# Performance work log

Hardware: AMD Instinct MI355X
Metric: run time of the kernel (lower is better)

Reference implementation:

```python
import jax, jax.numpy as jnp
import numpy as np

N_NODES = 100000
N_EDGES = 3200000
N_GRAPHS = 1024
IN_DIM, HID, OUT = 1, 32, 32
BN_EPS = 1e-5


def setup_inputs() -> dict:
    key = jax.random.key(0)
    ks = jax.random.split(key, 12)
    inp = {
        "x": jax.random.normal(ks[0], (N_NODES, IN_DIM), dtype=jnp.float32),
        "edge_index": jax.random.randint(ks[1], (2, N_EDGES), 0, N_NODES, dtype=jnp.int64),
        "batch": jnp.sort(jax.random.randint(ks[2], (N_NODES,), 0, N_GRAPHS, dtype=jnp.int64)),
        # GCNConv linear weights (out = x @ W + b) and BatchNorm (eval-mode) params
        "W1": jax.random.normal(ks[3], (IN_DIM, HID), dtype=jnp.float32) / np.sqrt(IN_DIM),
        "b1": jnp.zeros((HID,), jnp.float32),
        "bn1_g": jnp.ones((HID,), jnp.float32),
        "bn1_b": jnp.zeros((HID,), jnp.float32),
        "bn1_m": jax.random.normal(ks[4], (HID,), dtype=jnp.float32) * 0.1,
        "bn1_v": jnp.ones((HID,), jnp.float32),
        "W2": jax.random.normal(ks[5], (HID, HID), dtype=jnp.float32) / np.sqrt(HID),
        "b2": jnp.zeros((HID,), jnp.float32),
        "bn2_g": jnp.ones((HID,), jnp.float32),
        "bn2_b": jnp.zeros((HID,), jnp.float32),
        "bn2_m": jax.random.normal(ks[6], (HID,), dtype=jnp.float32) * 0.1,
        "bn2_v": jnp.ones((HID,), jnp.float32),
        "W3": jax.random.normal(ks[7], (HID, OUT), dtype=jnp.float32) / np.sqrt(HID),
        "b3": jnp.zeros((OUT,), jnp.float32),
    }
    return inp


def _gcn_norm(edge_index, n_nodes):
    # add self loops, compute sym-normalized edge weights (PyG GCNConv default)
    loop = jnp.arange(n_nodes, dtype=edge_index.dtype)
    src = jnp.concatenate([edge_index[0], loop])
    dst = jnp.concatenate([edge_index[1], loop])
    deg = jax.ops.segment_sum(jnp.ones_like(dst, dtype=jnp.float32), dst, num_segments=n_nodes)
    dinv = jnp.where(deg > 0, jax.lax.rsqrt(deg), 0.0)
    norm = dinv[src] * dinv[dst]  # [E + N]
    return src, dst, norm


def _gcn_conv(x, src, dst, norm, W, b, n_nodes):
    h = x @ W                                   # [N, F_out]
    msg = h[src] * norm[:, None]                # gather + scale, [E+N, F_out]
    out = jax.ops.segment_sum(msg, dst, num_segments=n_nodes)  # scatter-add
    return out + b


def _bn_eval(x, g, b, m, v):
    return (x - m) * jax.lax.rsqrt(v + BN_EPS) * g + b


def reference(x, edge_index, batch, W1, b1, bn1_g, bn1_b, bn1_m, bn1_v,
              W2, b2, bn2_g, bn2_b, bn2_m, bn2_v, W3, b3):
    n = x.shape[0]
    src, dst, norm = _gcn_norm(edge_index, n)
    h = _gcn_conv(x, src, dst, norm, W1, b1, n)
    h = jax.nn.relu(_bn_eval(h, bn1_g, bn1_b, bn1_m, bn1_v))  # dropout = id (eval)
    h = _gcn_conv(h, src, dst, norm, W2, b2, n)
    h = jax.nn.relu(_bn_eval(h, bn2_g, bn2_b, bn2_m, bn2_v))
    h = _gcn_conv(h, src, dst, norm, W3, b3, n)
    # global mean pool over graphs
    sums = jax.ops.segment_sum(h, batch, num_segments=N_GRAPHS)
    cnts = jax.ops.segment_sum(jnp.ones((n,), h.dtype), batch, num_segments=N_GRAPHS)
    return sums / jnp.maximum(cnts, 1.0)[:, None]
```

## Files before the change

kernel.cpp:

```cpp
#include <hip/hip_runtime.h>

#define N_NODES 100000
#define N_EDGES 3200000
#define N_GRAPHS 1024
#define HID 32
#define BN_EPS 1e-5f
#define NB 256

#define NBKT 512
#define NPB 196
#define PART_TILE 4096
#define PART_THREADS 256
#define PART_EPT (PART_TILE / PART_THREADS)


__device__ __forceinline__ int lbound(const int* __restrict__ a, int n, int key) {
    int lo = 0, hi = n;
    while (lo < hi) {
        int mid = (lo + hi) >> 1;
        if (a[mid] < key) lo = mid + 1; else hi = mid;
    }
    return lo;
}

__device__ __forceinline__ float bf2f(unsigned short h) {
    return __uint_as_float((unsigned)h << 16);
}
__device__ __forceinline__ unsigned short f2bf(float x) {
    unsigned u = __float_as_uint(x);
    u += 0x7fffu + ((u >> 16) & 1u);
    return (unsigned short)(u >> 16);
}


__global__ void k_zero(int* __restrict__ bhist) {
    bhist[threadIdx.x] = 0;
}

__global__ void k_hist(const int* __restrict__ dst, int* __restrict__ bhist) {
    __shared__ int h[NBKT];
    for (int i = threadIdx.x; i < NBKT; i += NB) h[i] = 0;
    __syncthreads();
    for (int e = blockIdx.x * NB + threadIdx.x; e < N_EDGES; e += gridDim.x * NB)
        atomicAdd(&h[__builtin_nontemporal_load(&dst[e]) / NPB], 1);
    __syncthreads();
    for (int i = threadIdx.x; i < NBKT; i += NB)
        if (h[i]) atomicAdd(&bhist[i], h[i]);
}

__global__ void k_scan512(const int* __restrict__ bhist, int* __restrict__ bstart,
                          int* __restrict__ bcursor) {
    __shared__ int sm[NBKT];
    int t = threadIdx.x;
    int orig = bhist[t];
    sm[t] = orig;
    __syncthreads();
    for (int off = 1; off < NBKT; off <<= 1) {
        int v = (t >= off) ? sm[t - off] : 0;
        __syncthreads();
        sm[t] += v;
        __syncthreads();
    }
    int ex = sm[t] - orig;
    bstart[t] = ex;
    bcursor[t] = ex;
    if (t == NBKT - 1) bstart[NBKT] = sm[t];
}

__global__ void k_partition(const int* __restrict__ src, const int* __restrict__ dst,
                            int* __restrict__ bcursor, unsigned* __restrict__ ebuf) {
    __shared__ int lh[NBKT];
    __shared__ int lcur[NBKT];
    const int tile0 = blockIdx.x * PART_TILE;
    for (int i = threadIdx.x; i < NBKT; i += PART_THREADS) lh[i] = 0;
    __syncthreads();
    int s[PART_EPT], bk[PART_EPT], dl[PART_EPT];
#pragma unroll
    for (int k = 0; k < PART_EPT; ++k) {
        int e = tile0 + k * PART_THREADS + threadIdx.x;
        bool ok = (e < N_EDGES);
        int sv = ok ? __builtin_nontemporal_load(&src[e]) : 0;
        int dv = ok ? __builtin_nontemporal_load(&dst[e]) : 0;
        s[k] = sv;
        bk[k] = ok ? (dv / NPB) : -1;
        dl[k] = dv - bk[k] * NPB;
        if (ok) atomicAdd(&lh[bk[k]], 1);
    }
    __syncthreads();
    for (int i = threadIdx.x; i < NBKT; i += PART_THREADS)
        lcur[i] = lh[i] ? atomicAdd(&bcursor[i], lh[i]) : 0;
    __syncthreads();
#pragma unroll
    for (int k = 0; k < PART_EPT; ++k) {
        if (bk[k] >= 0) {
            int pos = atomicAdd(&lcur[bk[k]], 1);
            ebuf[pos] = ((unsigned)dl[k] << 17) | (unsigned)s[k];
        }
    }
}

__global__ void k_bucket(const int* __restrict__ bstart,
                         const unsigned* __restrict__ ebuf,
                         const float* __restrict__ x,
                         int* __restrict__ rowstart, int* __restrict__ deg,
                         float* __restrict__ dinv, float* __restrict__ zs1,
                         int* __restrict__ csr) {
    __shared__ int hist[NPB];
    __shared__ int sm[256];
    __shared__ int lcur[NPB];
    const int b = blockIdx.x;
    const int node0 = b * NPB;
    const int nn = N_NODES - node0;
    const int elo = bstart[b], ehi = bstart[b + 1];
    const int t = threadIdx.x;

    for (int i = t; i < NPB; i += blockDim.x) hist[i] = 0;
    __syncthreads();
    for (int e = elo + t; e < ehi; e += blockDim.x)
        atomicAdd(&hist[ebuf[e] >> 17], 1);
    __syncthreads();
    int orig = 0;
    if (t < 256) { orig = (t < NPB) ? hist[t] : 0; sm[t] = orig; }
    __syncthreads();
    for (int off = 1; off < 256; off <<= 1) {
        int v = 0;
        if (t < 256 && t >= off) v = sm[t - off];
        __syncthreads();
        if (t < 256) sm[t] += v;
        __syncthreads();
    }
    if (t < NPB) {
        int ex = sm[t] - orig;
        lcur[t] = ex;
        if (t < nn) {
            int node = node0 + t;
            rowstart[node] = elo + ex;
            deg[node] = orig;
            float di = rsqrtf((float)(orig + 1));
            dinv[node] = di;
            zs1[node] = di * x[node];
        }
    }
    __syncthreads();
    for (int e = elo + t; e < ehi; e += blockDim.x) {
        unsigned pk = ebuf[e];
        int pos = atomicAdd(&lcur[pk >> 17], 1);
        csr[elo + pos] = (int)(pk & 0x1FFFFu);
    }
}


__global__ void k_gather1(const int* __restrict__ rowstart, const int* __restrict__ deg,
                          const int* __restrict__ csr, const float* __restrict__ dinv,
                          const float* __restrict__ zs1, float2* __restrict__ sd) {
    int v = blockIdx.x * NB + threadIdx.x;
    if (v < N_NODES) {
        int lo = rowstart[v], n = deg[v];
        float acc = zs1[v];
        int j = 0;
        for (; j + 4 <= n; j += 4) {
            int u0 = __builtin_nontemporal_load(&csr[lo + j]);
            int u1 = __builtin_nontemporal_load(&csr[lo + j + 1]);
            int u2 = __builtin_nontemporal_load(&csr[lo + j + 2]);
            int u3 = __builtin_nontemporal_load(&csr[lo + j + 3]);
            float a0 = zs1[u0], a1 = zs1[u1], a2 = zs1[u2], a3 = zs1[u3];
            acc += (a0 + a1) + (a2 + a3);
        }
        for (; j < n; ++j) acc += zs1[csr[lo + j]];
        float di = dinv[v];
        sd[v] = make_float2(di * acc, di);
    }
}

__global__ void k_gather2(const int* __restrict__ rowstart, const int* __restrict__ deg,
                          const int* __restrict__ csr, const float2* __restrict__ sd,
                          const float* __restrict__ W1, const float* __restrict__ b1,
                          const float* __restrict__ g1, const float* __restrict__ bb1,
                          const float* __restrict__ m1, const float* __restrict__ v1,
                          const float* __restrict__ W2,
                          const float* __restrict__ b2, const float* __restrict__ g2,
                          const float* __restrict__ bb2, const float* __restrict__ m2,
                          const float* __restrict__ v2, unsigned short* __restrict__ zs3h) {
    __shared__ float Ws[HID * HID];
    __shared__ float rowbuf[NB / HID][HID + 1];
    for (int k = threadIdx.x; k < HID * HID; k += NB) Ws[k] = W2[k];

    int t = blockIdx.x * NB + threadIdx.x;
    int v = t >> 5, f = t & 31, r = threadIdx.x >> 5;
    float sc1 = g1[f] * rsqrtf(v1[f] + BN_EPS);
    float A = W1[f] * sc1;
    float Bc = (b1[f] - m1[f]) * sc1 + bb1[f];
    float acc = 0.0f, di = 0.0f;
    if (v < N_NODES) {
        float2 pv = sd[v];
        di = pv.y;
        acc = di * fmaxf(pv.x * A + Bc, 0.0f);
        int lo = rowstart[v], n = deg[v];
        int j = 0;
        for (; j + 8 <= n; j += 8) {
            int u0 = __builtin_nontemporal_load(&csr[lo + j]);
            int u1 = __builtin_nontemporal_load(&csr[lo + j + 1]);
            int u2 = __builtin_nontemporal_load(&csr[lo + j + 2]);
            int u3 = __builtin_nontemporal_load(&csr[lo + j + 3]);
            int u4 = __builtin_nontemporal_load(&csr[lo + j + 4]);
            int u5 = __builtin_nontemporal_load(&csr[lo + j + 5]);
            int u6 = __builtin_nontemporal_load(&csr[lo + j + 6]);
            int u7 = __builtin_nontemporal_load(&csr[lo + j + 7]);
            float2 p0 = sd[u0], p1 = sd[u1], p2 = sd[u2], p3 = sd[u3];
            float2 p4 = sd[u4], p5 = sd[u5], p6 = sd[u6], p7 = sd[u7];
            float a0 = p0.y * fmaxf(p0.x * A + Bc, 0.0f);
            float a1 = p1.y * fmaxf(p1.x * A + Bc, 0.0f);
            float a2 = p2.y * fmaxf(p2.x * A + Bc, 0.0f);
            float a3 = p3.y * fmaxf(p3.x * A + Bc, 0.0f);
            float a4 = p4.y * fmaxf(p4.x * A + Bc, 0.0f);
            float a5 = p5.y * fmaxf(p5.x * A + Bc, 0.0f);
            float a6 = p6.y * fmaxf(p6.x * A + Bc, 0.0f);
            float a7 = p7.y * fmaxf(p7.x * A + Bc, 0.0f);
            acc += ((a0 + a1) + (a2 + a3)) + ((a4 + a5) + (a6 + a7));
        }
        for (; j < n; ++j) {
            float2 p = sd[csr[lo + j]];
            acc += p.y * fmaxf(p.x * A + Bc, 0.0f);
        }
        acc *= di;
    }
    rowbuf[r][f] = acc;
    __syncthreads();
    if (v < N_NODES) {
        float h = b2[f];
#pragma unroll
        for (int k = 0; k < HID; ++k) h += rowbuf[r][k] * Ws[k * HID + f];
        float sc2 = g2[f] * rsqrtf(v2[f] + BN_EPS);
        float z = fmaxf((h - m2[f]) * sc2 + bb2[f], 0.0f);
        zs3h[v * HID + f] = f2bf(di * z);
    }
}


__global__ void k_gather3(const int* __restrict__ rowstart, const int* __restrict__ deg,
                          const int* __restrict__ csr, const float* __restrict__ dinv,
                          const unsigned short* __restrict__ zs3h,
                          unsigned short* __restrict__ agg3h) {
    int t = blockIdx.x * NB + threadIdx.x;
    int v = t >> 5, f = t & 31;
    if (v < N_NODES) {
        int lo = rowstart[v], n = deg[v];
        float acc = bf2f(zs3h[v * HID + f]);
        int j = 0;
        for (; j + 8 <= n; j += 8) {
            int u0 = __builtin_nontemporal_load(&csr[lo + j]);
            int u1 = __builtin_nontemporal_load(&csr[lo + j + 1]);
            int u2 = __builtin_nontemporal_load(&csr[lo + j + 2]);
            int u3 = __builtin_nontemporal_load(&csr[lo + j + 3]);
            int u4 = __builtin_nontemporal_load(&csr[lo + j + 4]);
            int u5 = __builtin_nontemporal_load(&csr[lo + j + 5]);
            int u6 = __builtin_nontemporal_load(&csr[lo + j + 6]);
            int u7 = __builtin_nontemporal_load(&csr[lo + j + 7]);
            float a0 = bf2f(zs3h[u0 * HID + f]);
            float a1 = bf2f(zs3h[u1 * HID + f]);
            float a2 = bf2f(zs3h[u2 * HID + f]);
            float a3 = bf2f(zs3h[u3 * HID + f]);
            float a4 = bf2f(zs3h[u4 * HID + f]);
            float a5 = bf2f(zs3h[u5 * HID + f]);
            float a6 = bf2f(zs3h[u6 * HID + f]);
            float a7 = bf2f(zs3h[u7 * HID + f]);
            acc += ((a0 + a1) + (a2 + a3)) + ((a4 + a5) + (a6 + a7));
        }
        for (; j < n; ++j) acc += bf2f(zs3h[csr[lo + j] * HID + f]);
        __builtin_nontemporal_store(f2bf(dinv[v] * acc), &agg3h[v * HID + f]);
    }
}


__global__ void k_pool(const unsigned short* __restrict__ agg3h,
                       const int* __restrict__ batch,
                       const float* __restrict__ W3, const float* __restrict__ b3,
                       float* __restrict__ out) {
    __shared__ float Ws[HID * HID];
    __shared__ float part[NB / HID][HID + 1];
    __shared__ float mrow[HID];
    int g = blockIdx.x;
    for (int k = threadIdx.x; k < HID * HID; k += NB) Ws[k] = W3[k];

    int lo = lbound(batch, N_NODES, g);
    int hi = lbound(batch, N_NODES, g + 1);

    int r = threadIdx.x >> 5, f = threadIdx.x & 31;
    float acc = 0.0f;
    for (int i = lo + r; i < hi; i += NB / HID)
        acc += bf2f(__builtin_nontemporal_load(&agg3h[i * HID + f]));
    part[r][f] = acc;
    __syncthreads();
    if (threadIdx.x < HID) {
        float srow = 0.0f;
#pragma unroll
        for (int k = 0; k < NB / HID; ++k) srow += part[k][threadIdx.x];
        float c = (float)(hi - lo);
        mrow[threadIdx.x] = (hi > lo) ? srow / c : 0.0f;
    }
    __syncthreads();
    if (threadIdx.x < HID) {
        int ff = threadIdx.x;
        float o = 0.0f;
        if (hi > lo) {
            o = b3[ff];
#pragma unroll
            for (int k = 0; k < HID; ++k) o += mrow[k] * Ws[k * HID + ff];
        }
        out[g * HID + ff] = o;
    }
}


extern "C" void kernel_launch(void* const* d_in, const int* in_sizes, int n_in,
                              void* d_out, int out_size, void* d_ws, size_t ws_size,
                              hipStream_t stream) {
    const float* x     = (const float*)d_in[0];
    const int*   eidx  = (const int*)d_in[1];
    const int*   batch = (const int*)d_in[2];
    const float* W1    = (const float*)d_in[3];
    const float* b1    = (const float*)d_in[4];
    const float* bn1g  = (const float*)d_in[5];
    const float* bn1b  = (const float*)d_in[6];
    const float* bn1m  = (const float*)d_in[7];
    const float* bn1v  = (const float*)d_in[8];
    const float* W2    = (const float*)d_in[9];
    const float* b2    = (const float*)d_in[10];
    const float* bn2g  = (const float*)d_in[11];
    const float* bn2b  = (const float*)d_in[12];
    const float* bn2m  = (const float*)d_in[13];
    const float* bn2v  = (const float*)d_in[14];
    const float* W3    = (const float*)d_in[15];
    const float* b3    = (const float*)d_in[16];
    float* out = (float*)d_out;

    const int* src = eidx;
    const int* dst = eidx + N_EDGES;

    char* ws = (char*)d_ws;
    size_t off = 0;
    auto carve = [&](size_t bytes) {
        void* p = ws + off;
        off += (bytes + 255) & ~size_t(255);
        return p;
    };
    int*    bhist    = (int*)carve(NBKT * 4);
    int*    bstart   = (int*)carve((NBKT + 1) * 4);
    int*    bcursor  = (int*)carve(NBKT * 4);
    int*    rowstart = (int*)carve(N_NODES * 4);
    int*    deg      = (int*)carve(N_NODES * 4);
    float*  dinv     = (float*)carve(N_NODES * 4);
    float*  zs1      = (float*)carve(N_NODES * 4);
    float2* sd       = (float2*)carve((size_t)N_NODES * 8);
    int*    csr      = (int*)carve((size_t)N_EDGES * 4);
    char*   region   = (char*)carve((size_t)N_EDGES * 4);
    unsigned*       ebuf  = (unsigned*)region;
    unsigned short* zs3h  = (unsigned short*)region;
    unsigned short* agg3h = (unsigned short*)(region + (size_t)N_NODES * HID * 2);

    const int gN    = (N_NODES + NB - 1) / NB;
    const int gNF   = (N_NODES * HID + NB - 1) / NB;
    const int gPart = (N_EDGES + PART_TILE - 1) / PART_TILE;

    k_zero<<<1, NBKT, 0, stream>>>(bhist);
    k_hist<<<1024, NB, 0, stream>>>(dst, bhist);
    k_scan512<<<1, NBKT, 0, stream>>>(bhist, bstart, bcursor);
    k_partition<<<gPart, PART_THREADS, 0, stream>>>(src, dst, bcursor, ebuf);
    k_bucket<<<NBKT, 512, 0, stream>>>(bstart, ebuf, x, rowstart, deg, dinv, zs1, csr);
    k_gather1<<<gN, NB, 0, stream>>>(rowstart, deg, csr, dinv, zs1, sd);
    k_gather2<<<gNF, NB, 0, stream>>>(rowstart, deg, csr, sd,
                                      W1, b1, bn1g, bn1b, bn1m, bn1v,
                                      W2, b2, bn2g, bn2b, bn2m, bn2v, zs3h);
    k_gather3<<<gNF, NB, 0, stream>>>(rowstart, deg, csr, dinv, zs3h, agg3h);
    k_pool<<<N_GRAPHS, NB, 0, stream>>>(agg3h, batch, W3, b3, out);
}
```

Measured before the change: 296.2 us.

## Rework layer-2 gather to one wavefront per node with shuffle-broadcast edge loads

The second-layer gather now assigns a full 64-lane wavefront to each node instead of 32 threads per node. Each lane loads one neighbor's (s, dinv) pair, and the wave broadcasts the pairs with shuffles so every feature lane accumulates its share. Each half-wave handles half the edges, and the two halves are combined with an xor-shuffle. The W2 matvec now reads its inputs through shuffles rather than a shared row buffer. This removes the 32x redundant per-feature loads of csr and sd, at the cost of twice as many threads, 64 shuffles per 64-edge chunk, and idle lanes for low-degree nodes.

```diff
diff --git a/kernel.cpp b/kernel.cpp
--- a/kernel.cpp
+++ b/kernel.cpp
@@ -182,58 +182,51 @@
                           const float* __restrict__ bb2, const float* __restrict__ m2,
                           const float* __restrict__ v2, unsigned short* __restrict__ zs3h) {
     __shared__ float Ws[HID * HID];
-    __shared__ float rowbuf[NB / HID][HID + 1];
     for (int k = threadIdx.x; k < HID * HID; k += NB) Ws[k] = W2[k];
-
-    int t = blockIdx.x * NB + threadIdx.x;
-    int v = t >> 5, f = t & 31, r = threadIdx.x >> 5;
-    float sc1 = g1[f] * rsqrtf(v1[f] + BN_EPS);
-    float A = W1[f] * sc1;
-    float Bc = (b1[f] - m1[f]) * sc1 + bb1[f];
-    float acc = 0.0f, di = 0.0f;
-    if (v < N_NODES) {
-        float2 pv = sd[v];
-        di = pv.y;
-        acc = di * fmaxf(pv.x * A + Bc, 0.0f);
-        int lo = rowstart[v], n = deg[v];
-        int j = 0;
-        for (; j + 8 <= n; j += 8) {
-            int u0 = __builtin_nontemporal_load(&csr[lo + j]);
-            int u1 = __builtin_nontemporal_load(&csr[lo + j + 1]);
-            int u2 = __builtin_nontemporal_load(&csr[lo + j + 2]);
-            int u3 = __builtin_nontemporal_load(&csr[lo + j + 3]);
-            int u4 = __builtin_nontemporal_load(&csr[lo + j + 4]);
-            int u5 = __builtin_nontemporal_load(&csr[lo + j + 5]);
-            int u6 = __builtin_nontemporal_load(&csr[lo + j + 6]);
-            int u7 = __builtin_nontemporal_load(&csr[lo + j + 7]);
-            float2 p0 = sd[u0], p1 = sd[u1], p2 = sd[u2], p3 = sd[u3];
-            float2 p4 = sd[u4], p5 = sd[u5], p6 = sd[u6], p7 = sd[u7];
-            float a0 = p0.y * fmaxf(p0.x * A + Bc, 0.0f);
-            float a1 = p1.y * fmaxf(p1.x * A + Bc, 0.0f);
-            float a2 = p2.y * fmaxf(p2.x * A + Bc, 0.0f);
-            float a3 = p3.y * fmaxf(p3.x * A + Bc, 0.0f);
-            float a4 = p4.y * fmaxf(p4.x * A + Bc, 0.0f);
-            float a5 = p5.y * fmaxf(p5.x * A + Bc, 0.0f);
-            float a6 = p6.y * fmaxf(p6.x * A + Bc, 0.0f);
-            float a7 = p7.y * fmaxf(p7.x * A + Bc, 0.0f);
-            acc += ((a0 + a1) + (a2 + a3)) + ((a4 + a5) + (a6 + a7));
-        }
-        for (; j < n; ++j) {
-            float2 p = sd[csr[lo + j]];
-            acc += p.y * fmaxf(p.x * A + Bc, 0.0f);
-        }
-        acc *= di;
-    }
-    rowbuf[r][f] = acc;
-    __syncthreads();
-    if (v < N_NODES) {
-        float h = b2[f];
-#pragma unroll
-        for (int k = 0; k < HID; ++k) h += rowbuf[r][k] * Ws[k * HID + f];
-        float sc2 = g2[f] * rsqrtf(v2[f] + BN_EPS);
-        float z = fmaxf((h - m2[f]) * sc2 + bb2[f], 0.0f);
-        zs3h[v * HID + f] = f2bf(di * z);
-    }
+    __syncthreads();
+
+    const int lane = threadIdx.x & 63;
+    const int f = lane & 31;
+    const int hbase = lane & 32;
+    const int v = (blockIdx.x * NB + threadIdx.x) >> 6;
+    if (v >= N_NODES) return;
+
+    const float sc1 = g1[f] * rsqrtf(v1[f] + BN_EPS);
+    const float A = W1[f] * sc1;
+    const float Bc = (b1[f] - m1[f]) * sc1 + bb1[f];
+
+    const float2 pv = sd[v];
+    const float di = pv.y;
+    const int lo = rowstart[v], n = deg[v];
+
+    float acc = 0.0f;
+    for (int base = 0; base < n; base += 64) {
+        int j = base + lane;
+        float s_l = 0.0f, d_l = 0.0f;
+        if (j < n) {
+            int u = __builtin_nontemporal_load(&csr[lo + j]);
+            float2 p = sd[u];
+            s_l = p.x; d_l = p.y;
+        }
+#pragma unroll
+        for (int k = 0; k < 32; ++k) {
+            float sk = __shfl(s_l, hbase + k, 64);
+            float dk = __shfl(d_l, hbase + k, 64);
+            acc += dk * fmaxf(sk * A + Bc, 0.0f);
+        }
+    }
+    acc += __shfl_xor(acc, 32, 64);
+    acc = di * (acc + di * fmaxf(pv.x * A + Bc, 0.0f));
+
+    float h = b2[f];
+#pragma unroll
+    for (int k = 0; k < 32; ++k) {
+        float rk = __shfl(acc, hbase + k, 64);
+        h += rk * Ws[k * HID + f];
+    }
+    float sc2 = g2[f] * rsqrtf(v2[f] + BN_EPS);
+    float z = fmaxf((h - m2[f]) * sc2 + bb2[f], 0.0f);
+    if (lane < 32) zs3h[v * HID + f] = f2bf(di * z);
 }
 
 
@@ -360,6 +353,7 @@
 
     const int gN    = (N_NODES + NB - 1) / NB;
     const int gNF   = (N_NODES * HID + NB - 1) / NB;
+    const int gW    = ((size_t)N_NODES * 64 + NB - 1) / NB;
     const int gPart = (N_EDGES + PART_TILE - 1) / PART_TILE;
 
     k_zero<<<1, NBKT, 0, stream>>>(bhist);
@@ -368,9 +362,9 @@
     k_partition<<<gPart, PART_THREADS, 0, stream>>>(src, dst, bcursor, ebuf);
     k_bucket<<<NBKT, 512, 0, stream>>>(bstart, ebuf, x, rowstart, deg, dinv, zs1, csr);
     k_gather1<<<gN, NB, 0, stream>>>(rowstart, deg, csr, dinv, zs1, sd);
-    k_gather2<<<gNF, NB, 0, stream>>>(rowstart, deg, csr, sd,
-                                      W1, b1, bn1g, bn1b, bn1m, bn1v,
-                                      W2, b2, bn2g, bn2b, bn2m, bn2v, zs3h);
+    k_gather2<<<gW, NB, 0, stream>>>(rowstart, deg, csr, sd,
+                                     W1, b1, bn1g, bn1b, bn1m, bn1v,
+                                     W2, b2, bn2g, bn2b, bn2m, bn2v, zs3h);
     k_gather3<<<gNF, NB, 0, stream>>>(rowstart, deg, csr, dinv, zs3h, agg3h);
     k_pool<<<N_GRAPHS, NB, 0, stream>>>(agg3h, batch, W3, b3, out);
 }
```

Measured after the change: 324.9 us. 9.7% more time.

## Stage gather2 neighbor data in LDS and split layer-3 gather into feature halves

Applied to the files above, without the earlier changes.

k_gather2 now has each block cooperatively load its 8 nodes' contiguous CSR neighbor range into shared memory once, so the 32 feature lanes no longer each re-read the same csr and sd entries from global memory. Layer-2 output is written as two 16-feature bf16 tables, and layer 3 aggregates each half in its own pass. The halves make each gather table smaller and more cache-resident, at the cost of reading the CSR twice and adding a launch and extra block syncs.

```diff
diff --git a/kernel.cpp b/kernel.cpp
--- a/kernel.cpp
+++ b/kernel.cpp
@@ -12,6 +12,9 @@
 #define PART_TILE 4096
 #define PART_THREADS 256
 #define PART_EPT (PART_TILE / PART_THREADS)
+
+#define G2_NODES 8
+#define G2_WCAP 2048
 
 
 __device__ __forceinline__ int lbound(const int* __restrict__ a, int n, int key) {
@@ -180,22 +183,92 @@
                           const float* __restrict__ W2,
                           const float* __restrict__ b2, const float* __restrict__ g2,
                           const float* __restrict__ bb2, const float* __restrict__ m2,
-                          const float* __restrict__ v2, unsigned short* __restrict__ zs3h) {
+                          const float* __restrict__ v2,
+                          unsigned short* __restrict__ zs3a,
+                          unsigned short* __restrict__ zs3b) {
     __shared__ float Ws[HID * HID];
-    __shared__ float rowbuf[NB / HID][HID + 1];
-    for (int k = threadIdx.x; k < HID * HID; k += NB) Ws[k] = W2[k];
-
-    int t = blockIdx.x * NB + threadIdx.x;
-    int v = t >> 5, f = t & 31, r = threadIdx.x >> 5;
-    float sc1 = g1[f] * rsqrtf(v1[f] + BN_EPS);
-    float A = W1[f] * sc1;
-    float Bc = (b1[f] - m1[f]) * sc1 + bb1[f];
-    float acc = 0.0f, di = 0.0f;
-    if (v < N_NODES) {
+    __shared__ float2 sde[G2_WCAP];
+    __shared__ float rowbuf[G2_NODES][HID + 1];
+    __shared__ int sb[2];
+    const int tid = threadIdx.x;
+    for (int k = tid; k < HID * HID; k += NB) Ws[k] = W2[k];
+
+    const int r = tid >> 5, f = tid & 31;
+    const int v = blockIdx.x * G2_NODES + r;
+    const bool valid = v < N_NODES;
+
+    if (tid == 0) {
+        int first = blockIdx.x * G2_NODES;
+        int last = min(first + G2_NODES - 1, N_NODES - 1);
+        sb[0] = rowstart[first];
+        sb[1] = rowstart[last] + deg[last];
+    }
+
+    const float sc1 = g1[f] * rsqrtf(v1[f] + BN_EPS);
+    const float A = W1[f] * sc1;
+    const float Bc = (b1[f] - m1[f]) * sc1 + bb1[f];
+
+    float di = 0.0f, acc = 0.0f;
+    int rs = 0, re = 0;
+    if (valid) {
+        rs = rowstart[v];
+        re = rs + deg[v];
         float2 pv = sd[v];
         di = pv.y;
         acc = di * fmaxf(pv.x * A + Bc, 0.0f);
+    }
+    __syncthreads();
+    const int blo = sb[0], bhi = sb[1];
+
+    for (int w = blo; w < bhi; w += G2_WCAP) {
+        const int wn = min(G2_WCAP, bhi - w);
+        for (int i = tid; i < wn; i += NB) {
+            int u = __builtin_nontemporal_load(&csr[w + i]);
+            sde[i] = sd[u];
+        }
+        __syncthreads();
+        int jlo = max(rs, w) - w;
+        int jhi = min(re, w + wn) - w;
+        int j = jlo;
+        for (; j + 4 <= jhi; j += 4) {
+            float2 p0 = sde[j], p1 = sde[j + 1], p2 = sde[j + 2], p3 = sde[j + 3];
+            float a0 = p0.y * fmaxf(p0.x * A + Bc, 0.0f);
+            float a1 = p1.y * fmaxf(p1.x * A + Bc, 0.0f);
+            float a2 = p2.y * fmaxf(p2.x * A + Bc, 0.0f);
+            float a3 = p3.y * fmaxf(p3.x * A + Bc, 0.0f);
+            acc += (a0 + a1) + (a2 + a3);
+        }
+        for (; j < jhi; ++j) {
+            float2 p = sde[j];
+            acc += p.y * fmaxf(p.x * A + Bc, 0.0f);
+        }
+        __syncthreads();
+    }
+    acc *= di;
+    rowbuf[r][f] = acc;
+    __syncthreads();
+    if (valid) {
+        float h = b2[f];
+#pragma unroll
+        for (int k = 0; k < HID; ++k) h += rowbuf[r][k] * Ws[k * HID + f];
+        float sc2 = g2[f] * rsqrtf(v2[f] + BN_EPS);
+        float z = fmaxf((h - m2[f]) * sc2 + bb2[f], 0.0f);
+        unsigned short o = f2bf(di * z);
+        if (f < 16) zs3a[v * 16 + f] = o;
+        else        zs3b[v * 16 + (f - 16)] = o;
+    }
+}
+
+
+__global__ void k_gather3h(const int* __restrict__ rowstart, const int* __restrict__ deg,
+                           const int* __restrict__ csr, const float* __restrict__ dinv,
+                           const unsigned short* __restrict__ tab,
+                           unsigned short* __restrict__ agg3h, int halfofs) {
+    int t = blockIdx.x * NB + threadIdx.x;
+    int v = t >> 4, f = t & 15;
+    if (v < N_NODES) {
         int lo = rowstart[v], n = deg[v];
+        float acc = bf2f(tab[v * 16 + f]);
         int j = 0;
         for (; j + 8 <= n; j += 8) {
             int u0 = __builtin_nontemporal_load(&csr[lo + j]);
@@ -206,68 +279,18 @@
             int u5 = __builtin_nontemporal_load(&csr[lo + j + 5]);
             int u6 = __builtin_nontemporal_load(&csr[lo + j + 6]);
             int u7 = __builtin_nontemporal_load(&csr[lo + j + 7]);
-            float2 p0 = sd[u0], p1 = sd[u1], p2 = sd[u2], p3 = sd[u3];
-            float2 p4 = sd[u4], p5 = sd[u5], p6 = sd[u6], p7 = sd[u7];
-            float a0 = p0.y * fmaxf(p0.x * A + Bc, 0.0f);
-            float a1 = p1.y * fmaxf(p1.x * A + Bc, 0.0f);
-            float a2 = p2.y * fmaxf(p2.x * A + Bc, 0.0f);
-            float a3 = p3.y * fmaxf(p3.x * A + Bc, 0.0f);
-            float a4 = p4.y * fmaxf(p4.x * A + Bc, 0.0f);
-            float a5 = p5.y * fmaxf(p5.x * A + Bc, 0.0f);
-            float a6 = p6.y * fmaxf(p6.x * A + Bc, 0.0f);
-            float a7 = p7.y * fmaxf(p7.x * A + Bc, 0.0f);
+            float a0 = bf2f(tab[u0 * 16 + f]);
+            float a1 = bf2f(tab[u1 * 16 + f]);
+            float a2 = bf2f(tab[u2 * 16 + f]);
+            float a3 = bf2f(tab[u3 * 16 + f]);
+            float a4 = bf2f(tab[u4 * 16 + f]);
+            float a5 = bf2f(tab[u5 * 16 + f]);
+            float a6 = bf2f(tab[u6 * 16 + f]);
+            float a7 = bf2f(tab[u7 * 16 + f]);
             acc += ((a0 + a1) + (a2 + a3)) + ((a4 + a5) + (a6 + a7));
         }
-        for (; j < n; ++j) {
-            float2 p = sd[csr[lo + j]];
-            acc += p.y * fmaxf(p.x * A + Bc, 0.0f);
-        }
-        acc *= di;
-    }
-    rowbuf[r][f] = acc;
-    __syncthreads();
-    if (v < N_NODES) {
-        float h = b2[f];
-#pragma unroll
-        for (int k = 0; k < HID; ++k) h += rowbuf[r][k] * Ws[k * HID + f];
-        float sc2 = g2[f] * rsqrtf(v2[f] + BN_EPS);
-        float z = fmaxf((h - m2[f]) * sc2 + bb2[f], 0.0f);
-        zs3h[v * HID + f] = f2bf(di * z);
-    }
-}
-
-
-__global__ void k_gather3(const int* __restrict__ rowstart, const int* __restrict__ deg,
-                          const int* __restrict__ csr, const float* __restrict__ dinv,
-                          const unsigned short* __restrict__ zs3h,
-                          unsigned short* __restrict__ agg3h) {
-    int t = blockIdx.x * NB + threadIdx.x;
-    int v = t >> 5, f = t & 31;
-    if (v < N_NODES) {
-        int lo = rowstart[v], n = deg[v];
-        float acc = bf2f(zs3h[v * HID + f]);
-        int j = 0;
-        for (; j + 8 <= n; j += 8) {
-            int u0 = __builtin_nontemporal_load(&csr[lo + j]);
-            int u1 = __builtin_nontemporal_load(&csr[lo + j + 1]);
-            int u2 = __builtin_nontemporal_load(&csr[lo + j + 2]);
-            int u3 = __builtin_nontemporal_load(&csr[lo + j + 3]);
-            int u4 = __builtin_nontemporal_load(&csr[lo + j + 4]);
-            int u5 = __builtin_nontemporal_load(&csr[lo + j + 5]);
-            int u6 = __builtin_nontemporal_load(&csr[lo + j + 6]);
-            int u7 = __builtin_nontemporal_load(&csr[lo + j + 7]);
-            float a0 = bf2f(zs3h[u0 * HID + f]);
-            float a1 = bf2f(zs3h[u1 * HID + f]);
-            float a2 = bf2f(zs3h[u2 * HID + f]);
-            float a3 = bf2f(zs3h[u3 * HID + f]);
-            float a4 = bf2f(zs3h[u4 * HID + f]);
-            float a5 = bf2f(zs3h[u5 * HID + f]);
-            float a6 = bf2f(zs3h[u6 * HID + f]);
-            float a7 = bf2f(zs3h[u7 * HID + f]);
-            acc += ((a0 + a1) + (a2 + a3)) + ((a4 + a5) + (a6 + a7));
-        }
-        for (; j < n; ++j) acc += bf2f(zs3h[csr[lo + j] * HID + f]);
-        __builtin_nontemporal_store(f2bf(dinv[v] * acc), &agg3h[v * HID + f]);
+        for (; j < n; ++j) acc += bf2f(tab[csr[lo + j] * 16 + f]);
+        __builtin_nontemporal_store(f2bf(dinv[v] * acc), &agg3h[v * HID + halfofs + f]);
     }
 }
 
@@ -355,11 +378,13 @@
     int*    csr      = (int*)carve((size_t)N_EDGES * 4);
     char*   region   = (char*)carve((size_t)N_EDGES * 4);
     unsigned*       ebuf  = (unsigned*)region;
-    unsigned short* zs3h  = (unsigned short*)region;
-    unsigned short* agg3h = (unsigned short*)(region + (size_t)N_NODES * HID * 2);
+    unsigned short* zs3a  = (unsigned short*)region;
+    unsigned short* zs3b  = (unsigned short*)(region + (size_t)N_NODES * 16 * 2);
+    unsigned short* agg3h = (unsigned short*)(region + (size_t)N_NODES * 32 * 2);
 
     const int gN    = (N_NODES + NB - 1) / NB;
-    const int gNF   = (N_NODES * HID + NB - 1) / NB;
+    const int gG2   = (N_NODES + G2_NODES - 1) / G2_NODES;
+    const int gG3   = (N_NODES * 16 + NB - 1) / NB;
     const int gPart = (N_EDGES + PART_TILE - 1) / PART_TILE;
 
     k_zero<<<1, NBKT, 0, stream>>>(bhist);
@@ -368,9 +393,10 @@
     k_partition<<<gPart, PART_THREADS, 0, stream>>>(src, dst, bcursor, ebuf);
     k_bucket<<<NBKT, 512, 0, stream>>>(bstart, ebuf, x, rowstart, deg, dinv, zs1, csr);
     k_gather1<<<gN, NB, 0, stream>>>(rowstart, deg, csr, dinv, zs1, sd);
-    k_gather2<<<gNF, NB, 0, stream>>>(rowstart, deg, csr, sd,
+    k_gather2<<<gG2, NB, 0, stream>>>(rowstart, deg, csr, sd,
                                       W1, b1, bn1g, bn1b, bn1m, bn1v,
-                                      W2, b2, bn2g, bn2b, bn2m, bn2v, zs3h);
-    k_gather3<<<gNF, NB, 0, stream>>>(rowstart, deg, csr, dinv, zs3h, agg3h);
+                                      W2, b2, bn2g, bn2b, bn2m, bn2v, zs3a, zs3b);
+    k_gather3h<<<gG3, NB, 0, stream>>>(rowstart, deg, csr, dinv, zs3a, agg3h, 0);
+    k_gather3h<<<gG3, NB, 0, stream>>>(rowstart, deg, csr, dinv, zs3b, agg3h, 16);
     k_pool<<<N_GRAPHS, NB, 0, stream>>>(agg3h, batch, W3, b3, out);
 }
```

New measurement: 267.4 us. 9.7% less time.
